# Kernel optimization log

Hardware: AMD Instinct MI355X
Metric: run time of the kernel (lower is better)

## Reference

```python
import jax, jax.numpy as jnp
import numpy as np

NB_BINS = 10
N = 33554432  # number of predictions


def setup_inputs() -> dict:
    key = jax.random.key(0)
    k1, k2 = jax.random.split(key)
    logits = jax.random.normal(k1, (N,), dtype=jnp.float32)
    labels = jax.random.randint(k2, (N,), 0, 2, dtype=jnp.int32)
    return {"logits": logits, "labels": labels}


def reference(logits, labels):
    nb = NB_BINS
    conf = jax.nn.sigmoid(logits)
    # Bin b covers (b/nb, (b+1)/nb]: conf > lower & conf <= upper.
    # ceil(conf*nb)-1 maps exact boundary k/nb to bin k-1, matching gt/le.
    # sigmoid output is strictly in (0,1) for finite logits, so clip is safe.
    bins = jnp.clip(jnp.ceil(conf * nb).astype(jnp.int32) - 1, 0, nb - 1)

    counts = jax.ops.segment_sum(jnp.ones_like(conf), bins, num_segments=nb)
    label_sum = jax.ops.segment_sum(labels.astype(conf.dtype), bins, num_segments=nb)
    conf_sum = jax.ops.segment_sum(conf, bins, num_segments=nb)

    nonempty = counts > 0
    denom = jnp.where(nonempty, counts, 1.0)
    positives_per_bin = jnp.where(nonempty, label_sum / denom, 0.0)
    confidence_per_bin = jnp.where(nonempty, conf_sum / denom, 0.0)

    ece_i = jnp.where(nonempty, jnp.abs(positives_per_bin - confidence_per_bin), 0.0)
    ece = jnp.sum(ece_i)
    max_ece = jnp.max(ece_i)  # original inits max_ece=0, zeros for empty bins match
    return positives_per_bin, confidence_per_bin, ece, max_ece
```

## Files before the change

kernel.cpp:

```cpp
#include <hip/hip_runtime.h>

#define NB 10
#define BLOCK 256
#define GRID 4096


__global__ __launch_bounds__(BLOCK) void ece_partial(const float* __restrict__ logits,
                                                     const int* __restrict__ labels,
                                                     unsigned int* __restrict__ ws,
                                                     int n, int wstride) {
    unsigned long long cnt64 = 0ULL, lab64 = 0ULL, rA = 0ULL, rB = 0ULL;

    const int tid = threadIdx.x;
    const int gtid = blockIdx.x * BLOCK + tid;
    const int n4 = n >> 2;
    const float4* __restrict__ l4 = (const float4*)logits;
    const int4*   __restrict__ b4 = (const int4*)labels;

    for (int v = gtid; v < n4; v += GRID * BLOCK) {
        float4 x = l4[v];
        int4  lb = b4[v];
#pragma unroll
        for (int j = 0; j < 4; ++j) {
            float xx = j == 0 ? x.x : j == 1 ? x.y : j == 2 ? x.z : x.w;
            unsigned ll = (unsigned)(j == 0 ? lb.x : j == 1 ? lb.y : j == 2 ? lb.z : lb.w);
            float e = __expf(-xx);
            float conf = __builtin_amdgcn_rcpf(1.0f + e);
            float t = conf * 10.0f;
            int b = (int)t;
            b = min(b, NB - 1);
            float r = t - (float)b;
            unsigned rfix = (unsigned)__builtin_fmaf(r, 63.0f, 0.5f);
            int s6 = b * 6;
            cnt64 += 1ULL << s6;
            lab64 += (unsigned long long)ll << s6;
            bool hi = b >= 5;
            int s12 = (hi ? b - 5 : b) * 12;
            unsigned long long val = (unsigned long long)rfix << s12;
            rA += hi ? 0ULL : val;
            rB += hi ? val : 0ULL;
        }
    }
    if (gtid == 0) {
        for (int j2 = n4 * 4; j2 < n; ++j2) {
            float e = __expf(-logits[j2]);
            float conf = __builtin_amdgcn_rcpf(1.0f + e);
            float t = conf * 10.0f;
            int b = (int)t;
            b = min(b, NB - 1);
            float r = t - (float)b;
            unsigned rfix = (unsigned)__builtin_fmaf(r, 63.0f, 0.5f);
            int s6 = b * 6;
            cnt64 += 1ULL << s6;
            lab64 += (unsigned long long)(unsigned)labels[j2] << s6;
            bool hi = b >= 5;
            int s12 = (hi ? b - 5 : b) * 12;
            unsigned long long val = (unsigned long long)rfix << s12;
            rA += hi ? 0ULL : val;
            rB += hi ? val : 0ULL;
        }
    }

    unsigned cl[NB], ru[NB];
#pragma unroll
    for (int i = 0; i < NB; ++i) {
        unsigned c = (unsigned)((cnt64 >> (6 * i)) & 63ULL);
        unsigned l = (unsigned)((lab64 >> (6 * i)) & 63ULL);
        cl[i] = c | (l << 16);
    }
#pragma unroll
    for (int i = 0; i < 5; ++i) {
        ru[i]     = (unsigned)((rA >> (12 * i)) & 4095ULL);
        ru[5 + i] = (unsigned)((rB >> (12 * i)) & 4095ULL);
    }

#pragma unroll
    for (int i = 0; i < NB; ++i) {
#pragma unroll
        for (int off = 32; off > 0; off >>= 1) {
            cl[i] += __shfl_down(cl[i], off, 64);
            ru[i] += __shfl_down(ru[i], off, 64);
        }
    }

    __shared__ unsigned red[4][2 * NB];
    const int wave = tid >> 6, lane = tid & 63;
    if (lane == 0) {
#pragma unroll
        for (int i = 0; i < NB; ++i) { red[wave][i] = cl[i]; red[wave][NB + i] = ru[i]; }
    }
    __syncthreads();
    if (tid < 2 * NB) {
        unsigned s = red[0][tid] + red[1][tid] + red[2][tid] + red[3][tid];
        if (tid < NB) {
            atomicAdd(&ws[tid * wstride], s & 0xffffu);
            atomicAdd(&ws[(NB + tid) * wstride], s >> 16);
        } else {
            atomicAdd(&ws[(NB + tid) * wstride], s);
        }
    }
}

__global__ void ece_final(const unsigned int* __restrict__ ws, float* __restrict__ out,
                          int wstride) {
    if (threadIdx.x == 0 && blockIdx.x == 0) {
        float ece = 0.0f, mx = 0.0f;
        for (int b = 0; b < NB; ++b) {
            unsigned cnt = ws[b * wstride];
            unsigned lab = ws[(NB + b) * wstride];
            unsigned rs  = ws[(2 * NB + b) * wstride];
            float pos = 0.0f, cfb = 0.0f, e = 0.0f;
            if (cnt > 0u) {
                float inv = 1.0f / (float)cnt;
                pos = (float)lab * inv;
                cfb = ((float)b + (float)rs * (1.0f / 63.0f) * inv) * 0.1f;
                e = fabsf(pos - cfb);
            }
            out[b] = pos;
            out[NB + b] = cfb;
            ece += e;
            mx = fmaxf(mx, e);
        }
        out[2 * NB] = ece;
        out[2 * NB + 1] = mx;
    }
}

extern "C" void kernel_launch(void* const* d_in, const int* in_sizes, int n_in,
                              void* d_out, int out_size, void* d_ws, size_t ws_size,
                              hipStream_t stream) {
    const float* logits = (const float*)d_in[0];
    const int*   labels = (const int*)d_in[1];
    float* out = (float*)d_out;
    unsigned int* ws = (unsigned int*)d_ws;
    int n = in_sizes[0];

    int wstride = (ws_size >= 30 * 16 * sizeof(unsigned)) ? 16 : 1;
    hipMemsetAsync(d_ws, 0, (size_t)(30 * wstride) * sizeof(unsigned), stream);

    ece_partial<<<GRID, BLOCK, 0, stream>>>(logits, labels, ws, n, wstride);
    ece_final<<<1, 64, 0, stream>>>(ws, out, wstride);
}
```

Measured before the change: 305.6 us.

## Batch four strided vector loads per iteration with periodic packed-counter flushes

Halves the grid so each thread processes more elements, and issues four float4 logit and label loads at once to raise memory-level parallelism. Uses nontemporal loads for streaming data. Packed 6-bit/12-bit counters are flushed into 32-bit accumulators every 8 vectors to avoid overflow with more elements per thread. Adds register pressure and extra unpack work per chunk.

```diff
diff --git a/kernel.cpp b/kernel.cpp
--- a/kernel.cpp
+++ b/kernel.cpp
@@ -2,76 +2,110 @@
 
 #define NB 10
 #define BLOCK 256
-#define GRID 4096
+#define GRID 2048
 
+
+typedef float vfloat4 __attribute__((ext_vector_type(4)));
+typedef int   vint4   __attribute__((ext_vector_type(4)));
+
+__device__ __forceinline__ void acc_one(float xx, unsigned ll,
+                                        unsigned long long& cnt64,
+                                        unsigned long long& lab64,
+                                        unsigned long long& rA,
+                                        unsigned long long& rB) {
+    float e = __expf(-xx);
+    float conf = __builtin_amdgcn_rcpf(1.0f + e);
+    float t = conf * 10.0f;
+    int b = (int)t;
+    b = min(b, NB - 1);
+    float r = t - (float)b;
+    unsigned rfix = (unsigned)__builtin_fmaf(r, 63.0f, 0.5f);
+    int s6 = b * 6;
+    cnt64 += 1ULL << s6;
+    lab64 += (unsigned long long)ll << s6;
+    bool hi = b >= 5;
+    int s12 = (hi ? b - 5 : b) * 12;
+    unsigned long long val = (unsigned long long)rfix << s12;
+    rA += hi ? 0ULL : val;
+    rB += hi ? val : 0ULL;
+}
+
+__device__ __forceinline__ void flush_packed(unsigned long long& cnt64,
+                                             unsigned long long& lab64,
+                                             unsigned long long& rA,
+                                             unsigned long long& rB,
+                                             unsigned* cl, unsigned* ru) {
+#pragma unroll
+    for (int i = 0; i < NB; ++i) {
+        unsigned c = (unsigned)((cnt64 >> (6 * i)) & 63ULL);
+        unsigned l = (unsigned)((lab64 >> (6 * i)) & 63ULL);
+        cl[i] += c | (l << 16);
+    }
+#pragma unroll
+    for (int i = 0; i < 5; ++i) {
+        ru[i]     += (unsigned)((rA >> (12 * i)) & 4095ULL);
+        ru[5 + i] += (unsigned)((rB >> (12 * i)) & 4095ULL);
+    }
+    cnt64 = 0ULL; lab64 = 0ULL; rA = 0ULL; rB = 0ULL;
+}
 
 __global__ __launch_bounds__(BLOCK) void ece_partial(const float* __restrict__ logits,
                                                      const int* __restrict__ labels,
                                                      unsigned int* __restrict__ ws,
                                                      int n, int wstride) {
-    unsigned long long cnt64 = 0ULL, lab64 = 0ULL, rA = 0ULL, rB = 0ULL;
-
     const int tid = threadIdx.x;
     const int gtid = blockIdx.x * BLOCK + tid;
     const int n4 = n >> 2;
-    const float4* __restrict__ l4 = (const float4*)logits;
-    const int4*   __restrict__ b4 = (const int4*)labels;
-
-    for (int v = gtid; v < n4; v += GRID * BLOCK) {
-        float4 x = l4[v];
-        int4  lb = b4[v];
-#pragma unroll
-        for (int j = 0; j < 4; ++j) {
-            float xx = j == 0 ? x.x : j == 1 ? x.y : j == 2 ? x.z : x.w;
-            unsigned ll = (unsigned)(j == 0 ? lb.x : j == 1 ? lb.y : j == 2 ? lb.z : lb.w);
-            float e = __expf(-xx);
-            float conf = __builtin_amdgcn_rcpf(1.0f + e);
-            float t = conf * 10.0f;
-            int b = (int)t;
-            b = min(b, NB - 1);
-            float r = t - (float)b;
-            unsigned rfix = (unsigned)__builtin_fmaf(r, 63.0f, 0.5f);
-            int s6 = b * 6;
-            cnt64 += 1ULL << s6;
-            lab64 += (unsigned long long)ll << s6;
-            bool hi = b >= 5;
-            int s12 = (hi ? b - 5 : b) * 12;
-            unsigned long long val = (unsigned long long)rfix << s12;
-            rA += hi ? 0ULL : val;
-            rB += hi ? val : 0ULL;
-        }
-    }
-    if (gtid == 0) {
-        for (int j2 = n4 * 4; j2 < n; ++j2) {
-            float e = __expf(-logits[j2]);
-            float conf = __builtin_amdgcn_rcpf(1.0f + e);
-            float t = conf * 10.0f;
-            int b = (int)t;
-            b = min(b, NB - 1);
-            float r = t - (float)b;
-            unsigned rfix = (unsigned)__builtin_fmaf(r, 63.0f, 0.5f);
-            int s6 = b * 6;
-            cnt64 += 1ULL << s6;
-            lab64 += (unsigned long long)(unsigned)labels[j2] << s6;
-            bool hi = b >= 5;
-            int s12 = (hi ? b - 5 : b) * 12;
-            unsigned long long val = (unsigned long long)rfix << s12;
-            rA += hi ? 0ULL : val;
-            rB += hi ? val : 0ULL;
-        }
-    }
+    const int S = GRID * BLOCK;
+    const vfloat4* __restrict__ l4 = (const vfloat4*)logits;
+    const vint4*   __restrict__ b4 = (const vint4*)labels;
 
     unsigned cl[NB], ru[NB];
 #pragma unroll
-    for (int i = 0; i < NB; ++i) {
-        unsigned c = (unsigned)((cnt64 >> (6 * i)) & 63ULL);
-        unsigned l = (unsigned)((lab64 >> (6 * i)) & 63ULL);
-        cl[i] = c | (l << 16);
+    for (int i = 0; i < NB; ++i) { cl[i] = 0u; ru[i] = 0u; }
+
+    int v = gtid;
+    while (v < n4) {
+        unsigned long long cnt64 = 0ULL, lab64 = 0ULL, rA = 0ULL, rB = 0ULL;
+        int done = 0;
+        while (done < 8 && v + 3 * S < n4) {
+            vfloat4 x0 = __builtin_nontemporal_load(&l4[v]);
+            vfloat4 x1 = __builtin_nontemporal_load(&l4[v + S]);
+            vfloat4 x2 = __builtin_nontemporal_load(&l4[v + 2 * S]);
+            vfloat4 x3 = __builtin_nontemporal_load(&l4[v + 3 * S]);
+            vint4   y0 = __builtin_nontemporal_load(&b4[v]);
+            vint4   y1 = __builtin_nontemporal_load(&b4[v + S]);
+            vint4   y2 = __builtin_nontemporal_load(&b4[v + 2 * S]);
+            vint4   y3 = __builtin_nontemporal_load(&b4[v + 3 * S]);
+            v += 4 * S;
+            done += 4;
+#pragma unroll
+            for (int j = 0; j < 4; ++j) acc_one(x0[j], (unsigned)y0[j], cnt64, lab64, rA, rB);
+#pragma unroll
+            for (int j = 0; j < 4; ++j) acc_one(x1[j], (unsigned)y1[j], cnt64, lab64, rA, rB);
+#pragma unroll
+            for (int j = 0; j < 4; ++j) acc_one(x2[j], (unsigned)y2[j], cnt64, lab64, rA, rB);
+#pragma unroll
+            for (int j = 0; j < 4; ++j) acc_one(x3[j], (unsigned)y3[j], cnt64, lab64, rA, rB);
+        }
+        while (done < 8 && v < n4) {
+            vfloat4 x = __builtin_nontemporal_load(&l4[v]);
+            vint4   y = __builtin_nontemporal_load(&b4[v]);
+            v += S;
+            done += 1;
+#pragma unroll
+            for (int j = 0; j < 4; ++j) acc_one(x[j], (unsigned)y[j], cnt64, lab64, rA, rB);
+        }
+        flush_packed(cnt64, lab64, rA, rB, cl, ru);
     }
-#pragma unroll
-    for (int i = 0; i < 5; ++i) {
-        ru[i]     = (unsigned)((rA >> (12 * i)) & 4095ULL);
-        ru[5 + i] = (unsigned)((rB >> (12 * i)) & 4095ULL);
+    if (gtid == 0 && (n & 3)) {
+        unsigned long long cnt64 = 0ULL, lab64 = 0ULL, rA = 0ULL, rB = 0ULL;
+        for (int j2 = n4 * 4; j2 < n; ++j2) {
+            acc_one(__builtin_nontemporal_load(&logits[j2]),
+                    (unsigned)__builtin_nontemporal_load(&labels[j2]),
+                    cnt64, lab64, rA, rB);
+        }
+        flush_packed(cnt64, lab64, rA, rB, cl, ru);
     }
 
 #pragma unroll
```

New measurement: 279.8 us. 8.4% less time.
